# Performance work log

Hardware: AMD Instinct MI355X
Metric: run time of the kernel (lower is better)

## Reference

```python
import jax, jax.numpy as jnp
import numpy as np

# Circuit dimensions: B batch, N sum nodes (rows), C child nodes (cols), NSE stored edges.
B, N, C, NSE = 256, 8192, 32768, 524288


def setup_inputs() -> dict:
    key = jax.random.key(0)
    k1, k2, k3, k4 = jax.random.split(key, 4)
    # child log-likelihoods (output of child_layer.log_likelihood_of_nodes), [B, C]
    child_ll = jax.random.normal(k1, (B, C), dtype=jnp.float32) - 2.0
    # BCOO .data of the (unnormalized) log weights, [NSE]
    log_w_data = jax.random.normal(k2, (NSE,), dtype=jnp.float32)
    # BCOO indices[:, 0]: parent sum-node row of each edge. Guarantee every row
    # appears at least once so no node is empty (log(0) avoided), then sort
    # (matching .sort_indices() row-major ordering).
    rows = jnp.sort(jnp.concatenate([
        jnp.arange(N, dtype=jnp.int32),
        jax.random.randint(k3, (NSE - N,), 0, N, dtype=jnp.int32),
    ]))
    # BCOO indices[:, 1]: child node column of each edge
    cols = jax.random.randint(k4, (NSE,), 0, C, dtype=jnp.int32)
    return {"child_ll": child_ll, "log_w_data": log_w_data,
            "rows": rows, "cols": cols, "n_nodes": N}


def reference(child_ll, log_w_data, rows, cols, n_nodes):
    # log normalization constants per node (max-stabilized, as in
    # SparseSumLayer.log_normalization_constants)
    m = log_w_data.max()
    z = m + jnp.log(jax.ops.segment_sum(jnp.exp(log_w_data - m), rows,
                                        num_segments=n_nodes))  # [N]
    # per-edge: exp(log_w + child_ll[col])  (as in log_likelihood_of_nodes_single)
    vals = jnp.exp(log_w_data[None, :] + child_ll[:, cols])        # [B, NSE]
    # row-wise sparse sum (BCOO .sum(1).todense())
    summed = jax.ops.segment_sum(vals.T, rows, num_segments=n_nodes).T  # [B, N]
    # normalized log-likelihood of each sum node
    return jnp.log(summed) - z[None, :]
```

## Files before the change

### kernel.cpp

```cpp
#include <hip/hip_runtime.h>
#include <hip/hip_bf16.h>

#define BB   256
#define NN   8192
#define CC   32768
#define NSE_ 524288
#define GB   64
#define PREP_BLOCKS ((NSE_ + 64 + 255) / 256)
#define TP_BLOCKS   ((CC / 64) * 4)

typedef float v2f __attribute__((ext_vector_type(2)));

#define FP8_SCALE  8.0f
#define LOG_SCALE  2.0794415416798357f

__device__ __forceinline__ unsigned int pack4_fp8(float a, float b, float c,
                                                  float d) {
    int v = __builtin_amdgcn_cvt_pk_fp8_f32(a, b, 0, false);
    v = __builtin_amdgcn_cvt_pk_fp8_f32(c, d, v, true);
    return (unsigned)v;
}

__global__ __launch_bounds__(256) void prep_transpose_kernel(
    const float* __restrict__ lw, const int* __restrict__ rows,
    const int* __restrict__ cols, const float* __restrict__ ll,
    uint2* __restrict__ cw, int* __restrict__ rs,
    unsigned char* __restrict__ cet) {
    int bid = blockIdx.x;
    int t = threadIdx.x;
    if (bid < PREP_BLOCKS) {
        int e = bid * 256 + t;
        if (e < NSE_) {
            cw[e] = make_uint2((unsigned)cols[e],
                               __float_as_uint(__expf(lw[e])));
            if (e == 0) { rs[0] = 0; rs[NN] = NSE_; }
            else if (rows[e] != rows[e - 1]) rs[rows[e]] = e;
        } else if (e < NSE_ + 64) {
            cw[e] = make_uint2(0u, 0u);
        }
        return;
    }
    bid -= PREP_BLOCKS;
    int g = bid & 3;
    int ct = bid >> 2;
    int c0 = ct * 64, b0 = g * GB;
    __shared__ float tile[64][65];
    #pragma unroll
    for (int k = 0; k < 4; ++k) {
        int row = (t >> 4) + 16 * k;
        int c4 = t & 15;
        const float4 v = *reinterpret_cast<const float4*>(
            ll + (size_t)(b0 + row) * CC + c0 + 4 * c4);
        tile[c4 * 4 + 0][row] = v.x;
        tile[c4 * 4 + 1][row] = v.y;
        tile[c4 * 4 + 2][row] = v.z;
        tile[c4 * 4 + 3][row] = v.w;
    }
    __syncthreads();
    {
        int cl = t >> 2, q = t & 3;
        unsigned int o[4];
        #pragma unroll
        for (int i = 0; i < 4; ++i) {
            int b = q * 16 + i * 4;
            o[i] = pack4_fp8(__expf(tile[cl][b + 0]) * FP8_SCALE,
                             __expf(tile[cl][b + 1]) * FP8_SCALE,
                             __expf(tile[cl][b + 2]) * FP8_SCALE,
                             __expf(tile[cl][b + 3]) * FP8_SCALE);
        }
        uint4 u4 = make_uint4(o[0], o[1], o[2], o[3]);
        *reinterpret_cast<uint4*>(
            cet + ((size_t)g * CC + c0 + cl) * GB + q * 16) = u4;
    }
}

__global__ __launch_bounds__(256) void sum_rows_kernel(
    const uint2* __restrict__ cw, const int* __restrict__ rs,
    const uint4* __restrict__ cet, float* __restrict__ out) {
    __shared__ uint2 stage[4][64];
    __shared__ float lds_out[64][17];
    int g = blockIdx.x & 3;
    int ntile = blockIdx.x >> 2;
    int n0 = ntile * 16;
    int wv = threadIdx.x >> 6;
    int lane = threadIdx.x & 63;
    int grp = lane >> 2;
    int bq = lane & 3;
    const uint4* slice = cet + (size_t)g * CC * 4;
    uint2* st = stage[wv];

    for (int r = 0; r < 4; ++r) {
        int n = n0 + wv * 4 + r;
        int s = __builtin_amdgcn_readfirstlane(rs[n]);
        int t = __builtin_amdgcn_readfirstlane(rs[n + 1]);
        v2f acc[8];
        #pragma unroll
        for (int k = 0; k < 8; ++k) acc[k] = 0.f;
        float zs = 0.f;
        uint2 v = cw[s + lane];
        int eb = s;
        for (; eb + 64 <= t; eb += 64) {
            st[lane] = v;
            v = cw[eb + 64 + lane];
            #pragma unroll
            for (int j = 0; j < 4; ++j) {
                uint2 p = st[j * 16 + grp];
                float w = __uint_as_float(p.y);
                uint4 u = slice[(p.x << 2) | bq];
                v2f w2; w2.x = w; w2.y = w;
                acc[0] += w2 * __builtin_amdgcn_cvt_pk_f32_fp8(u.x, false);
                acc[1] += w2 * __builtin_amdgcn_cvt_pk_f32_fp8(u.x, true);
                acc[2] += w2 * __builtin_amdgcn_cvt_pk_f32_fp8(u.y, false);
                acc[3] += w2 * __builtin_amdgcn_cvt_pk_f32_fp8(u.y, true);
                acc[4] += w2 * __builtin_amdgcn_cvt_pk_f32_fp8(u.z, false);
                acc[5] += w2 * __builtin_amdgcn_cvt_pk_f32_fp8(u.z, true);
                acc[6] += w2 * __builtin_amdgcn_cvt_pk_f32_fp8(u.w, false);
                acc[7] += w2 * __builtin_amdgcn_cvt_pk_f32_fp8(u.w, true);
                zs += w;
            }
        }
        int rem = t - eb;
        if (rem > 0) {
            if (eb + lane >= t) v.y = 0u;
            st[lane] = v;
            int msteps = (rem + 15) >> 4;
            for (int j = 0; j < msteps; ++j) {
                uint2 p = st[j * 16 + grp];
                float w = __uint_as_float(p.y);
                uint4 u = slice[(p.x << 2) | bq];
                v2f w2; w2.x = w; w2.y = w;
                acc[0] += w2 * __builtin_amdgcn_cvt_pk_f32_fp8(u.x, false);
                acc[1] += w2 * __builtin_amdgcn_cvt_pk_f32_fp8(u.x, true);
                acc[2] += w2 * __builtin_amdgcn_cvt_pk_f32_fp8(u.y, false);
                acc[3] += w2 * __builtin_amdgcn_cvt_pk_f32_fp8(u.y, true);
                acc[4] += w2 * __builtin_amdgcn_cvt_pk_f32_fp8(u.z, false);
                acc[5] += w2 * __builtin_amdgcn_cvt_pk_f32_fp8(u.z, true);
                acc[6] += w2 * __builtin_amdgcn_cvt_pk_f32_fp8(u.w, false);
                acc[7] += w2 * __builtin_amdgcn_cvt_pk_f32_fp8(u.w, true);
                zs += w;
            }
        }
        #pragma unroll
        for (int off = 4; off <= 32; off <<= 1) {
            #pragma unroll
            for (int k = 0; k < 8; ++k) {
                acc[k].x += __shfl_xor(acc[k].x, off);
                acc[k].y += __shfl_xor(acc[k].y, off);
            }
            zs += __shfl_xor(zs, off);
        }
        if (grp == 0) {
            float lz = __logf(zs) + LOG_SCALE;
            int col = wv * 4 + r;
            #pragma unroll
            for (int k = 0; k < 8; ++k) {
                lds_out[bq * 16 + 2 * k + 0][col] = __logf(acc[k].x) - lz;
                lds_out[bq * 16 + 2 * k + 1][col] = __logf(acc[k].y) - lz;
            }
        }
    }
    __syncthreads();
    {
        int bl = threadIdx.x >> 2, ch = threadIdx.x & 3;
        float4 o = make_float4(lds_out[bl][ch * 4 + 0], lds_out[bl][ch * 4 + 1],
                               lds_out[bl][ch * 4 + 2], lds_out[bl][ch * 4 + 3]);
        *reinterpret_cast<float4*>(
            out + (size_t)(g * GB + bl) * NN + n0 + ch * 4) = o;
    }
}

extern "C" void kernel_launch(void* const* d_in, const int* in_sizes, int n_in,
                              void* d_out, int out_size, void* d_ws, size_t ws_size,
                              hipStream_t stream) {
    const float* child_ll = (const float*)d_in[0];
    const float* log_w    = (const float*)d_in[1];
    const int*   rows     = (const int*)  d_in[2];
    const int*   cols     = (const int*)  d_in[3];
    float* out = (float*)d_out;

    char* ws = (char*)d_ws;
    uint2*         cwp = (uint2*)ws;
    int*           rs  = (int*)(ws + (size_t)5 * 1024 * 1024);
    unsigned char* cet = (unsigned char*)(ws + (size_t)6 * 1024 * 1024);

    prep_transpose_kernel<<<PREP_BLOCKS + TP_BLOCKS, 256, 0, stream>>>(
        log_w, rows, cols, child_ll, cwp, rs, cet);
    sum_rows_kernel<<<(NN / 16) * 4, 256, 0, stream>>>(
        cwp, rs, (const uint4*)cet, out);
}
```

Baseline: 122.4 us.

## Prefetch edge batches in registers and reduce partial sums through LDS

```diff
diff --git a/kernel.cpp b/kernel.cpp
--- a/kernel.cpp
+++ b/kernel.cpp
@@ -1,5 +1,4 @@
 #include <hip/hip_runtime.h>
-#include <hip/hip_bf16.h>
 
 #define BB   256
 #define NN   8192
@@ -41,7 +40,7 @@
         return;
     }
     bid -= PREP_BLOCKS;
-    int g = bid & 3;
+    int g = (bid + 1) & 3;
     int ct = bid >> 2;
     int c0 = ct * 64, b0 = g * GB;
     __shared__ float tile[64][65];
@@ -77,7 +76,7 @@
 __global__ __launch_bounds__(256) void sum_rows_kernel(
     const uint2* __restrict__ cw, const int* __restrict__ rs,
     const uint4* __restrict__ cet, float* __restrict__ out) {
-    __shared__ uint2 stage[4][64];
+    __shared__ __align__(16) float red[4][16][20];
     __shared__ float lds_out[64][17];
     int g = blockIdx.x & 3;
     int ntile = blockIdx.x >> 2;
@@ -87,78 +86,112 @@
     int grp = lane >> 2;
     int bq = lane & 3;
     const uint4* slice = cet + (size_t)g * CC * 4;
-    uint2* st = stage[wv];
-
+
+#define ACC(w_, u_) do {                                                   \
+        v2f w2v; w2v.x = (w_); w2v.y = (w_);                               \
+        acc[0] += w2v * __builtin_amdgcn_cvt_pk_f32_fp8((u_).x, false);    \
+        acc[1] += w2v * __builtin_amdgcn_cvt_pk_f32_fp8((u_).x, true);     \
+        acc[2] += w2v * __builtin_amdgcn_cvt_pk_f32_fp8((u_).y, false);    \
+        acc[3] += w2v * __builtin_amdgcn_cvt_pk_f32_fp8((u_).y, true);     \
+        acc[4] += w2v * __builtin_amdgcn_cvt_pk_f32_fp8((u_).z, false);    \
+        acc[5] += w2v * __builtin_amdgcn_cvt_pk_f32_fp8((u_).z, true);     \
+        acc[6] += w2v * __builtin_amdgcn_cvt_pk_f32_fp8((u_).w, false);    \
+        acc[7] += w2v * __builtin_amdgcn_cvt_pk_f32_fp8((u_).w, true);     \
+        zs += (w_);                                                        \
+    } while (0)
+
+    int myrs = 0;
+    if (lane < 5) myrs = rs[n0 + wv * 4 + lane];
+    int s = __builtin_amdgcn_readfirstlane(__shfl(myrs, 0));
+
+    uint2 pa = cw[s + grp];
+    uint2 pb = cw[s + 16 + grp];
+    uint2 pc = cw[s + 32 + grp];
+    uint2 pd = cw[s + 48 + grp];
+
+    #pragma unroll
     for (int r = 0; r < 4; ++r) {
-        int n = n0 + wv * 4 + r;
-        int s = __builtin_amdgcn_readfirstlane(rs[n]);
-        int t = __builtin_amdgcn_readfirstlane(rs[n + 1]);
+        int t = __builtin_amdgcn_readfirstlane(__shfl(myrs, r + 1));
         v2f acc[8];
         #pragma unroll
         for (int k = 0; k < 8; ++k) acc[k] = 0.f;
         float zs = 0.f;
-        uint2 v = cw[s + lane];
         int eb = s;
         for (; eb + 64 <= t; eb += 64) {
-            st[lane] = v;
-            v = cw[eb + 64 + lane];
-            #pragma unroll
-            for (int j = 0; j < 4; ++j) {
-                uint2 p = st[j * 16 + grp];
-                float w = __uint_as_float(p.y);
-                uint4 u = slice[(p.x << 2) | bq];
-                v2f w2; w2.x = w; w2.y = w;
-                acc[0] += w2 * __builtin_amdgcn_cvt_pk_f32_fp8(u.x, false);
-                acc[1] += w2 * __builtin_amdgcn_cvt_pk_f32_fp8(u.x, true);
-                acc[2] += w2 * __builtin_amdgcn_cvt_pk_f32_fp8(u.y, false);
-                acc[3] += w2 * __builtin_amdgcn_cvt_pk_f32_fp8(u.y, true);
-                acc[4] += w2 * __builtin_amdgcn_cvt_pk_f32_fp8(u.z, false);
-                acc[5] += w2 * __builtin_amdgcn_cvt_pk_f32_fp8(u.z, true);
-                acc[6] += w2 * __builtin_amdgcn_cvt_pk_f32_fp8(u.w, false);
-                acc[7] += w2 * __builtin_amdgcn_cvt_pk_f32_fp8(u.w, true);
-                zs += w;
-            }
+            unsigned c0 = pa.x, c1 = pb.x, c2 = pc.x, c3 = pd.x;
+            float w0 = __uint_as_float(pa.y), w1 = __uint_as_float(pb.y);
+            float w2s = __uint_as_float(pc.y), w3 = __uint_as_float(pd.y);
+            uint4 u0 = slice[(c0 << 2) | bq];
+            uint4 u1 = slice[(c1 << 2) | bq];
+            uint4 u2 = slice[(c2 << 2) | bq];
+            uint4 u3 = slice[(c3 << 2) | bq];
+            pa = cw[eb + 64 + grp];
+            pb = cw[eb + 80 + grp];
+            pc = cw[eb + 96 + grp];
+            pd = cw[eb + 112 + grp];
+            ACC(w0, u0);
+            ACC(w1, u1);
+            ACC(w2s, u2);
+            ACC(w3, u3);
         }
         int rem = t - eb;
         if (rem > 0) {
-            if (eb + lane >= t) v.y = 0u;
-            st[lane] = v;
-            int msteps = (rem + 15) >> 4;
-            for (int j = 0; j < msteps; ++j) {
-                uint2 p = st[j * 16 + grp];
-                float w = __uint_as_float(p.y);
-                uint4 u = slice[(p.x << 2) | bq];
-                v2f w2; w2.x = w; w2.y = w;
-                acc[0] += w2 * __builtin_amdgcn_cvt_pk_f32_fp8(u.x, false);
-                acc[1] += w2 * __builtin_amdgcn_cvt_pk_f32_fp8(u.x, true);
-                acc[2] += w2 * __builtin_amdgcn_cvt_pk_f32_fp8(u.y, false);
-                acc[3] += w2 * __builtin_amdgcn_cvt_pk_f32_fp8(u.y, true);
-                acc[4] += w2 * __builtin_amdgcn_cvt_pk_f32_fp8(u.z, false);
-                acc[5] += w2 * __builtin_amdgcn_cvt_pk_f32_fp8(u.z, true);
-                acc[6] += w2 * __builtin_amdgcn_cvt_pk_f32_fp8(u.w, false);
-                acc[7] += w2 * __builtin_amdgcn_cvt_pk_f32_fp8(u.w, true);
-                zs += w;
+            float w = (grp < rem) ? __uint_as_float(pa.y) : 0.f;
+            uint4 u = slice[(pa.x << 2) | bq];
+            ACC(w, u);
+            if (rem > 16) {
+                w = (grp + 16 < rem) ? __uint_as_float(pb.y) : 0.f;
+                u = slice[(pb.x << 2) | bq];
+                ACC(w, u);
             }
-        }
-        #pragma unroll
-        for (int off = 4; off <= 32; off <<= 1) {
-            #pragma unroll
-            for (int k = 0; k < 8; ++k) {
-                acc[k].x += __shfl_xor(acc[k].x, off);
-                acc[k].y += __shfl_xor(acc[k].y, off);
+            if (rem > 32) {
+                w = (grp + 32 < rem) ? __uint_as_float(pc.y) : 0.f;
+                u = slice[(pc.x << 2) | bq];
+                ACC(w, u);
             }
-            zs += __shfl_xor(zs, off);
-        }
-        if (grp == 0) {
+            if (rem > 48) {
+                w = (grp + 48 < rem) ? __uint_as_float(pd.y) : 0.f;
+                u = slice[(pd.x << 2) | bq];
+                ACC(w, u);
+            }
+        }
+        if (r < 3) {
+            pa = cw[t + grp];
+            pb = cw[t + 16 + grp];
+            pc = cw[t + 32 + grp];
+            pd = cw[t + 48 + grp];
+        }
+        #pragma unroll
+        for (int k = 0; k < 8; ++k) {
+            acc[k].x += __shfl_xor(acc[k].x, 16);
+            acc[k].y += __shfl_xor(acc[k].y, 16);
+        }
+        #pragma unroll
+        for (int k = 0; k < 8; ++k) {
+            acc[k].x += __shfl_xor(acc[k].x, 32);
+            acc[k].y += __shfl_xor(acc[k].y, 32);
+        }
+        zs += __shfl_xor(zs, 4);
+        zs += __shfl_xor(zs, 8);
+        zs += __shfl_xor(zs, 16);
+        zs += __shfl_xor(zs, 32);
+        if (lane < 16) {
+            float4* dst = reinterpret_cast<float4*>(&red[wv][lane][0]);
+            dst[0] = make_float4(acc[0].x, acc[0].y, acc[1].x, acc[1].y);
+            dst[1] = make_float4(acc[2].x, acc[2].y, acc[3].x, acc[3].y);
+            dst[2] = make_float4(acc[4].x, acc[4].y, acc[5].x, acc[5].y);
+            dst[3] = make_float4(acc[6].x, acc[6].y, acc[7].x, acc[7].y);
+        }
+        {
+            int bq16 = lane >> 4, e16 = lane & 15;
+            float sum = red[wv][bq16][e16] + red[wv][4 + bq16][e16]
+                      + red[wv][8 + bq16][e16] + red[wv][12 + bq16][e16];
             float lz = __logf(zs) + LOG_SCALE;
-            int col = wv * 4 + r;
-            #pragma unroll
-            for (int k = 0; k < 8; ++k) {
-                lds_out[bq * 16 + 2 * k + 0][col] = __logf(acc[k].x) - lz;
-                lds_out[bq * 16 + 2 * k + 1][col] = __logf(acc[k].y) - lz;
-            }
-        }
-    }
+            lds_out[lane][wv * 4 + r] = __logf(sum) - lz;
+        }
+        s = t;
+    }
+#undef ACC
     __syncthreads();
     {
         int bl = threadIdx.x >> 2, ch = threadIdx.x & 3;
```

After: 110.8 us. 9.5% less time.
